# Performance work log

Measured on AMD Instinct MI355X. Metric: run time of the kernel, lower is better.

Reference implementation:

```python
import math
import jax, jax.numpy as jnp
import numpy as np

H = 1024          # hidden size
NH = 16           # num attention heads
HD = H // NH      # head dim = 64
MAXPOS = 1024
HYP_W = 0.5


def setup_inputs() -> dict:
    key = jax.random.key(0)
    ks = jax.random.split(key, 9)
    B, S = 4, 1024
    scale = 1.0 / math.sqrt(H)
    return {
        "hidden_states": jax.random.normal(ks[0], (B, S, H), jnp.float32),
        "attention_mask": jnp.zeros((B, 1, 1, S), jnp.float32),
        "hyperbolic_attention_scores": jax.random.normal(ks[1], (B, S, S), jnp.float32),
        "Wq": jax.random.normal(ks[2], (H, H), jnp.float32) * scale,
        "bq": jnp.zeros((H,), jnp.float32),
        "Wk": jax.random.normal(ks[3], (H, H), jnp.float32) * scale,
        "bk": jnp.zeros((H,), jnp.float32),
        "Wv": jax.random.normal(ks[4], (H, H), jnp.float32) * scale,
        "bv": jnp.zeros((H,), jnp.float32),
        "dist_emb": jax.random.normal(ks[5], (2 * MAXPOS - 1, HD), jnp.float32) * 0.02,
    }


def reference(hidden_states, attention_mask, hyperbolic_attention_scores,
              Wq, bq, Wk, bk, Wv, bv, dist_emb):
    B, S, _ = hidden_states.shape

    def split_heads(x):  # [B,S,H] -> [B,NH,S,HD]
        return x.reshape(B, S, NH, HD).transpose(0, 2, 1, 3)

    q = split_heads(hidden_states @ Wq + bq)
    k = split_heads(hidden_states @ Wk + bk)
    v = split_heads(hidden_states @ Wv + bv)

    # raw scores [B,NH,Sq,Sk]
    scores = jnp.einsum("bhqd,bhkd->bhqk", q, k)

    # relative_key_query position bias
    distance = jnp.arange(S)[:, None] - jnp.arange(S)[None, :]  # [Sq,Sk]
    pe = dist_emb[distance + MAXPOS - 1]                        # [Sq,Sk,HD]
    scores = scores + jnp.einsum("bhld,lrd->bhlr", q, pe)
    scores = scores + jnp.einsum("bhrd,lrd->bhlr", k, pe)

    scores = scores / math.sqrt(HD)
    scores = scores + HYP_W * hyperbolic_attention_scores[:, None, :, :]
    scores = scores + attention_mask

    probs = jax.nn.softmax(scores, axis=-1)
    ctx = jnp.einsum("bhqk,bhkd->bhqd", probs, v)  # [B,NH,S,HD]
    ctx = ctx.transpose(0, 2, 1, 3).reshape(B, S, H)
    return ctx
```

## Files before the change

kernel.cpp:

```cpp
#include <hip/hip_runtime.h>
#include <math.h>

#define S_SEQ 1024
#define NHEAD 16
#define HDIM  64
#define BATCH 4

typedef __attribute__((ext_vector_type(8))) short bf16x8;
typedef __attribute__((ext_vector_type(4))) float f32x4;

#define MFMA16 __builtin_amdgcn_mfma_f32_16x16x32_bf16

__device__ __forceinline__ float bf2f(unsigned short h) {
    union { unsigned u; float f; } un; un.u = ((unsigned)h) << 16; return un.f;
}
__device__ __forceinline__ unsigned short f2bf(float x) {
    union { float f; unsigned u; } un; un.f = x;
    unsigned r = un.u + 0x7FFFu + ((un.u >> 16) & 1u);
    return (unsigned short)(r >> 16);
}
__device__ __forceinline__ unsigned pack2bf(float a, float b) {
    return (unsigned)f2bf(a) | ((unsigned)f2bf(b) << 16);
}
__device__ __forceinline__ void glds16(const unsigned short* g, unsigned short* l) {
    __builtin_amdgcn_global_load_lds(
        (const __attribute__((address_space(1))) void*)g,
        (__attribute__((address_space(3))) void*)l, 16, 0, 0);
}

#define HS_F4 1048576
#define PE_F4 32752
#define CONV_BLKS ((HS_F4 + PE_F4 + 255) / 256)

__global__ __launch_bounds__(256) void prep_kernel(
    const float* __restrict__ hs, const float* __restrict__ de,
    const float* __restrict__ Wq, const float* __restrict__ Wk,
    const float* __restrict__ Wv,
    unsigned short* __restrict__ hsb, unsigned short* __restrict__ peb,
    unsigned short* __restrict__ wt)
{
    __shared__ float tl[64 * 67];
    const int bx = blockIdx.x;
    const int t = threadIdx.x;

    if (bx < CONV_BLKS) {
        int i = bx * 256 + t;
        if (i < HS_F4) {
            float4 v = ((const float4*)hs)[i];
            uint2 o;
            o.x = pack2bf(v.x, v.y);
            o.y = pack2bf(v.z, v.w);
            *(uint2*)(hsb + 4 * (size_t)i) = o;
        } else if (i < HS_F4 + PE_F4) {
            int j = i - HS_F4;
            float4 v = ((const float4*)de)[j];
            uint2 o;
            o.x = pack2bf(v.x, v.y);
            o.y = pack2bf(v.z, v.w);
            *(uint2*)(peb + 4 * (size_t)j) = o;
        }
        return;
    }

    const int id = bx - CONV_BLKS;
    const int which = id >> 8;
    const int rem = id & 255;
    const float* W = (which == 0) ? Wq : (which == 1) ? Wk : Wv;
    unsigned short* outp = wt + (size_t)which * 1024 * 1024;
    const int k0 = (rem >> 4) * 64, n0 = (rem & 15) * 64;

#pragma unroll
    for (int it = 0; it < 4; ++it) {
        int idx = t + it * 256;
        int kr = idx >> 4;
        int c4 = (idx & 15) << 2;
        float4 v = *(const float4*)(W + (size_t)(k0 + kr) * 1024 + n0 + c4);
        tl[kr * 67 + c4 + 0] = v.x; tl[kr * 67 + c4 + 1] = v.y;
        tl[kr * 67 + c4 + 2] = v.z; tl[kr * 67 + c4 + 3] = v.w;
    }
    __syncthreads();
#pragma unroll
    for (int it = 0; it < 2; ++it) {
        int idx = t + it * 256;
        int nr = idx >> 3;
        int k8 = (idx & 7) << 3;
        unsigned short r[8];
#pragma unroll
        for (int e = 0; e < 8; ++e) r[e] = f2bf(tl[(k8 + e) * 67 + nr]);
        uint4 o;
        o.x = (unsigned)r[0] | ((unsigned)r[1] << 16);
        o.y = (unsigned)r[2] | ((unsigned)r[3] << 16);
        o.z = (unsigned)r[4] | ((unsigned)r[5] << 16);
        o.w = (unsigned)r[6] | ((unsigned)r[7] << 16);
        *(uint4*)(outp + (size_t)(n0 + nr) * 1024 + k0 + k8) = o;
    }
}

__global__ __launch_bounds__(256, 3) void qkv_mfma_kernel(
    const unsigned short* __restrict__ hsb, const unsigned short* __restrict__ wt,
    const float* __restrict__ bq, const float* __restrict__ bk,
    const float* __restrict__ bv,
    unsigned short* __restrict__ qo, unsigned short* __restrict__ ko,
    unsigned short* __restrict__ vo)
{
    __shared__ unsigned short As[128 * 64];
    __shared__ unsigned short Bs[128 * 64];

    const int t = threadIdx.x;
    const int lane = t & 63, w = t >> 6;
    const int l16 = lane & 15, quad = lane >> 4;
    const int wm = w >> 1, wn = w & 1;
    const int lrow = lane >> 3, cs = lane & 7;

    const int lid = blockIdx.x + 8 * blockIdx.y + 256 * blockIdx.z;
    const int x = lid & 7, pos = lid >> 3;
    const int pl = pos / 24, sub = pos - pl * 24;
    const int m0 = (4 * x + pl) * 128;
    const int which = sub >> 3;
    const int n0 = (sub & 7) * 128;

    const unsigned short* wts = wt + (size_t)which * 1024 * 1024;
    const float* bias = (which == 0) ? bq : (which == 1) ? bk : bv;

    f32x4 acc[4][4];
#pragma unroll
    for (int i = 0; i < 4; ++i)
#pragma unroll
        for (int j = 0; j < 4; ++j) acc[i][j] = (f32x4){0.f, 0.f, 0.f, 0.f};

    for (int kk = 0; kk < 1024; kk += 64) {
#pragma unroll
        for (int it = 0; it < 4; ++it) {
            int mrow = 32 * w + 8 * it + lrow;
            int kch = cs ^ (mrow & 7);
            glds16(hsb + (size_t)(m0 + mrow) * 1024 + kk + kch * 8,
                   &As[(32 * w + 8 * it) * 64]);
            glds16(wts + (size_t)(n0 + mrow) * 1024 + kk + kch * 8,
                   &Bs[(32 * w + 8 * it) * 64]);
        }
        __syncthreads();

        bf16x8 af[4][2], bf[4][2];
#pragma unroll
        for (int i = 0; i < 4; ++i) {
            int am = 64 * wm + 16 * i + l16;
            int base = am * 64;
            af[i][0] = *(bf16x8*)&As[base + ((quad ^ (am & 7)) << 3)];
            af[i][1] = *(bf16x8*)&As[base + (((quad + 4) ^ (am & 7)) << 3)];
        }
#pragma unroll
        for (int j = 0; j < 4; ++j) {
            int bn = 64 * wn + 16 * j + l16;
            int base = bn * 64;
            bf[j][0] = *(bf16x8*)&Bs[base + ((quad ^ (bn & 7)) << 3)];
            bf[j][1] = *(bf16x8*)&Bs[base + (((quad + 4) ^ (bn & 7)) << 3)];
        }
#pragma unroll
        for (int i = 0; i < 4; ++i)
#pragma unroll
            for (int j = 0; j < 4; ++j) {
                acc[i][j] = MFMA16(af[i][0], bf[j][0], acc[i][j], 0, 0, 0);
                acc[i][j] = MFMA16(af[i][1], bf[j][1], acc[i][j], 0, 0, 0);
            }
        __syncthreads();
    }

    const float qs = (which == 0) ? 0.125f : 1.0f;
#pragma unroll
    for (int j = 0; j < 4; ++j) {
        int n = n0 + 64 * wn + 16 * j + l16;
        float bvv = bias[n];
        int hh = n >> 6, hd = n & 63;
#pragma unroll
        for (int i = 0; i < 4; ++i) {
            int mb = m0 + 64 * wm + 16 * i + 4 * quad;
            int bb = mb >> 10, s = mb & 1023;
            if (which == 2) {
                uint2 o;
                o.x = pack2bf(acc[i][j][0] + bvv, acc[i][j][1] + bvv);
                o.y = pack2bf(acc[i][j][2] + bvv, acc[i][j][3] + bvv);
                *(uint2*)(vo + ((size_t)(bb * NHEAD + hh) * HDIM + hd) * S_SEQ + s) = o;
            } else {
                unsigned short* outp = (which == 0) ? qo : ko;
#pragma unroll
                for (int r = 0; r < 4; ++r)
                    outp[((size_t)(bb * NHEAD + hh) * S_SEQ + s + r) * HDIM + hd] =
                        f2bf((acc[i][j][r] + bvv) * qs);
            }
        }
    }
}

__global__ __launch_bounds__(256, 4) void attn_mfma_kernel(
    const unsigned short* __restrict__ qw, const unsigned short* __restrict__ kw,
    const unsigned short* __restrict__ vtw, const unsigned short* __restrict__ peb,
    const float* __restrict__ hyp, const float* __restrict__ mask,
    float* __restrict__ out)
{
    __shared__ unsigned short pes[128 * 64];
    __shared__ unsigned short QDs[64 * 100];
    __shared__ unsigned short KDs[96 * 36];
    __shared__ unsigned short ps[64 * 32];

    const int t = threadIdx.x;
    const int lane = t & 63, w = t >> 6;
    const int l16 = lane & 15, quad = lane >> 4;
    const int lL = 16 * w + l16;
    const int l0 = blockIdx.x * 64;
    const int h = blockIdx.y, b = blockIdx.z;

    const unsigned short* qb = qw + ((size_t)(b * NHEAD + h) * S_SEQ + l0) * HDIM;
    const unsigned short* kb = kw + (size_t)(b * NHEAD + h) * S_SEQ * HDIM;
    const unsigned short* vtb = vtw + (size_t)(b * NHEAD + h) * HDIM * S_SEQ;
    const float* hypb = hyp + (size_t)b * S_SEQ * S_SEQ + (size_t)(l0 + lL) * S_SEQ;
    const float* maskb = mask + b * S_SEQ;

    const bf16x8 qf0 = *(const bf16x8*)(qb + lL * 64 + quad * 8);
    const bf16x8 qf1 = *(const bf16x8*)(qb + lL * 64 + 32 + quad * 8);

    const int pb0 = l0 + 992;
    int sbP = pb0 & 127;
    int sbQ = pb0 % 96;
    int cQ = (pb0 - lL) % 96;

    const int strow = t >> 3, stp = t & 7;
    const int swzl = (lL >> 1) & 3;

    const int fstart = (w < 2) ? 3 * w : 2 * w + 2;
    const int fcnt   = (w < 2) ? 3 : 2;

    f32x4 accO[4];
#pragma unroll
    for (int jf = 0; jf < 4; ++jf) accO[jf] = (f32x4){0.f, 0.f, 0.f, 0.f};
    float m_run = -INFINITY, lsum = 0.f;

#pragma unroll
    for (int it = 0; it < 2; ++it) {
        int idx = t + it * 256;
        int row = idx >> 3, p = idx & 7;
        int ar = pb0 + 32 + row;
        int slot = ar & 127;
        int src = ar > 2046 ? 2046 : ar;
        *(uint4*)&pes[slot * 64 + (p << 3)] =
            *(const uint4*)(peb + (size_t)src * 64 + ((p ^ (ar & 7)) << 3));
    }
    __syncthreads();

#pragma unroll
    for (int jd = 0; jd < 4; ++jd) {
        int s = (sbP + 32 + 16 * jd + l16) & 127;
        const int sw = s & 7;
        bf16x8 p0 = *(bf16x8*)&pes[s * 64 + ((quad ^ sw) << 3)];
        bf16x8 p1 = *(bf16x8*)&pes[s * 64 + (((quad + 4) ^ sw) << 3)];
        f32x4 aq = (f32x4){0.f, 0.f, 0.f, 0.f};
        aq = MFMA16(p0, qf0, aq, 0, 0, 0);
        aq = MFMA16(p1, qf1, aq, 0, 0, 0);
        int cb = cQ + 32 + 16 * jd + 4 * quad;
#pragma unroll
        for (int i = 0; i < 4; ++i) {
            int c = cb + i; if (c >= 96) c -= 96;
            QDs[lL * 100 + c] = f2bf(aq[i]);
        }
    }

    bf16x8 kfC0 = *(const bf16x8*)(kb + (size_t)l16 * 64 + quad * 8);
    bf16x8 kfC1 = *(const bf16x8*)(kb + (size_t)l16 * 64 + 32 + quad * 8);
    bf16x8 kfC2 = *(const bf16x8*)(kb + (size_t)(16 + l16) * 64 + quad * 8);
    bf16x8 kfC3 = *(const bf16x8*)(kb + (size_t)(16 + l16) * 64 + 32 + quad * 8);
    uint4 peReg;
    {
        int ar = pb0 + strow;
        peReg = *(const uint4*)(peb + (size_t)ar * 64 + ((stp ^ (ar & 7)) << 3));
    }

    for (int kt = 0; kt < 32; ++kt) {
        const int r0 = 32 * kt;

        const float4 hv0 = *(const float4*)(hypb + r0 + 4 * quad);
        const float4 hv1 = *(const float4*)(hypb + r0 + 16 + 4 * quad);
        const float4 mv0 = *(const float4*)(maskb + r0 + 4 * quad);
        const float4 mv1 = *(const float4*)(maskb + r0 + 16 + 4 * quad);

        {
            int slot = (sbP + strow) & 127;
            *(uint4*)&pes[slot * 64 + (stp << 3)] = peReg;
        }
        __syncthreads();

        __builtin_amdgcn_s_setprio(1);
        f32x4 accS0 = (f32x4){0.f, 0.f, 0.f, 0.f};
        f32x4 accS1 = (f32x4){0.f, 0.f, 0.f, 0.f};
        accS0 = MFMA16(kfC0, qf0, accS0, 0, 0, 0);
        accS0 = MFMA16(kfC1, qf1, accS0, 0, 0, 0);
        accS1 = MFMA16(kfC2, qf0, accS1, 0, 0, 0);
        accS1 = MFMA16(kfC3, qf1, accS1, 0, 0, 0);

#pragma unroll
        for (int jd = 0; jd < 2; ++jd) {
            int s = (sbP + 16 * jd + l16) & 127;
            const int sw = s & 7;
            bf16x8 p0 = *(bf16x8*)&pes[s * 64 + ((quad ^ sw) << 3)];
            bf16x8 p1 = *(bf16x8*)&pes[s * 64 + (((quad + 4) ^ sw) << 3)];
            f32x4 aq = (f32x4){0.f, 0.f, 0.f, 0.f};
            aq = MFMA16(p0, qf0, aq, 0, 0, 0);
            aq = MFMA16(p1, qf1, aq, 0, 0, 0);
            int cb = cQ + 16 * jd + 4 * quad;
#pragma unroll
            for (int i = 0; i < 4; ++i) {
                int c = cb + i; if (c >= 96) c -= 96;
                QDs[lL * 100 + c] = f2bf(aq[i]);
            }
        }

#pragma unroll
        for (int jk = 0; jk < 3; ++jk) {
            if (jk < fcnt) {
                const int f = fstart + jk;
                const int diB = 16 * ((f + 1) >> 1);
                const int rB = (f & 1) ? 0 : 16;
                int s = (sbP + diB + l16) & 127;
                const int sw = s & 7;
                bf16x8 p0 = *(bf16x8*)&pes[s * 64 + ((quad ^ sw) << 3)];
                bf16x8 p1 = *(bf16x8*)&pes[s * 64 + (((quad + 4) ^ sw) << 3)];
                f32x4 ak = (f32x4){0.f, 0.f, 0.f, 0.f};
                if (rB == 0) {
                    ak = MFMA16(p0, kfC0, ak, 0, 0, 0);
                    ak = MFMA16(p1, kfC1, ak, 0, 0, 0);
                } else {
                    ak = MFMA16(p0, kfC2, ak, 0, 0, 0);
                    ak = MFMA16(p1, kfC3, ak, 0, 0, 0);
                }
                const int colr = rB + l16;
                const int aB = diB + colr + 4 * quad - 16;
#pragma unroll
                for (int i = 0; i < 4; ++i)
                    KDs[(aB + i) * 36 + colr] = f2bf(ak[i] * 0.125f);
            }
        }
        __builtin_amdgcn_s_setprio(0);
        __syncthreads();

        {
            const int r0n = (kt < 31) ? r0 + 32 : r0;
            kfC0 = *(const bf16x8*)(kb + (size_t)(r0n + l16) * 64 + quad * 8);
            kfC1 = *(const bf16x8*)(kb + (size_t)(r0n + l16) * 64 + 32 + quad * 8);
            kfC2 = *(const bf16x8*)(kb + (size_t)(r0n + 16 + l16) * 64 + quad * 8);
            kfC3 = *(const bf16x8*)(kb + (size_t)(r0n + 16 + l16) * 64 + 32 + quad * 8);
            int ar = pb0 - r0n + strow;
            peReg = *(const uint4*)(peb + (size_t)ar * 64 + ((stp ^ (ar & 7)) << 3));
        }
        bf16x8 vvA[4];
#pragma unroll
        for (int jf = 0; jf < 4; ++jf)
            vvA[jf] = *(const bf16x8*)(vtb + (size_t)(16 * jf + l16) * S_SEQ +
                                       r0 + quad * 8);

        float sc0[4], sc1[4];
        {
            uint2 qd2 = *(uint2*)&QDs[lL * 100 + sbQ + 28 - 4 * quad];
            uint2 kd2 = *(uint2*)&KDs[(lL + 15) * 36 + 4 * quad];
            float hm0 = fmaf(0.5f, hv0.x, mv0.x);
            float hm1 = fmaf(0.5f, hv0.y, mv0.y);
            float hm2 = fmaf(0.5f, hv0.z, mv0.z);
            float hm3 = fmaf(0.5f, hv0.w, mv0.w);
            sc0[0] = accS0[0] + bf2f((unsigned short)(qd2.y >> 16)) +
                     bf2f((unsigned short)(kd2.x & 0xffff)) + hm0;
            sc0[1] = accS0[1] + bf2f((unsigned short)(qd2.y & 0xffff)) +
                     bf2f((unsigned short)(kd2.x >> 16)) + hm1;
            sc0[2] = accS0[2] + bf2f((unsigned short)(qd2.x >> 16)) +
                     bf2f((unsigned short)(kd2.y & 0xffff)) + hm2;
            sc0[3] = accS0[3] + bf2f((unsigned short)(qd2.x & 0xffff)) +
                     bf2f((unsigned short)(kd2.y >> 16)) + hm3;
        }
        {
            uint2 qd2 = *(uint2*)&QDs[lL * 100 + sbQ + 12 - 4 * quad];
            uint2 kd2 = *(uint2*)&KDs[(lL + 15) * 36 + 16 + 4 * quad];
            float hm0 = fmaf(0.5f, hv1.x, mv1.x);
            float hm1 = fmaf(0.5f, hv1.y, mv1.y);
            float hm2 = fmaf(0.5f, hv1.z, mv1.z);
            float hm3 = fmaf(0.5f, hv1.w, mv1.w);
            sc1[0] = accS1[0] + bf2f((unsigned short)(qd2.y >> 16)) +
                     bf2f((unsigned short)(kd2.x & 0xffff)) + hm0;
            sc1[1] = accS1[1] + bf2f((unsigned short)(qd2.y & 0xffff)) +
                     bf2f((unsigned short)(kd2.x >> 16)) + hm1;
            sc1[2] = accS1[2] + bf2f((unsigned short)(qd2.x >> 16)) +
                     bf2f((unsigned short)(kd2.y & 0xffff)) + hm2;
            sc1[3] = accS1[3] + bf2f((unsigned short)(qd2.x & 0xffff)) +
                     bf2f((unsigned short)(kd2.y >> 16)) + hm3;
        }

        float mx = fmaxf(fmaxf(fmaxf(sc0[0], sc0[1]), fmaxf(sc0[2], sc0[3])),
                         fmaxf(fmaxf(sc1[0], sc1[1]), fmaxf(sc1[2], sc1[3])));
        mx = fmaxf(mx, __shfl_xor(mx, 16));
        mx = fmaxf(mx, __shfl_xor(mx, 32));
        const float m_new = fmaxf(m_run, mx);
        const float al = __expf(m_run - m_new);
        m_run = m_new;
        float rs = 0.f;
#pragma unroll
        for (int i = 0; i < 4; ++i) { sc0[i] = __expf(sc0[i] - m_new); rs += sc0[i]; }
#pragma unroll
        for (int i = 0; i < 4; ++i) { sc1[i] = __expf(sc1[i] - m_new); rs += sc1[i]; }
        rs += __shfl_xor(rs, 16);
        rs += __shfl_xor(rs, 32);
        lsum = lsum * al + rs;

        {
            uint2 pw;
            pw.x = pack2bf(sc0[0], sc0[1]); pw.y = pack2bf(sc0[2], sc0[3]);
            *(uint2*)&ps[lL * 32 + (((quad >> 1) ^ swzl) << 3) + 4 * (quad & 1)] = pw;
            pw.x = pack2bf(sc1[0], sc1[1]); pw.y = pack2bf(sc1[2], sc1[3]);
            *(uint2*)&ps[lL * 32 + (((2 + (quad >> 1)) ^ swzl) << 3) + 4 * (quad & 1)] = pw;
        }

        const bf16x8 pf = *(const bf16x8*)&ps[lL * 32 + ((quad ^ swzl) << 3)];
        const float alv0 = __shfl(al, 4 * quad + 0);
        const float alv1 = __shfl(al, 4 * quad + 1);
        const float alv2 = __shfl(al, 4 * quad + 2);
        const float alv3 = __shfl(al, 4 * quad + 3);
#pragma unroll
        for (int jf = 0; jf < 4; ++jf) {
            f32x4 o = accO[jf];
            o[0] *= alv0; o[1] *= alv1; o[2] *= alv2; o[3] *= alv3;
            o = MFMA16(pf, vvA[jf], o, 0, 0, 0);
            accO[jf] = o;
        }

        sbP = (sbP - 32) & 127;
        sbQ -= 32; if (sbQ < 0) sbQ += 96;
        cQ -= 32; if (cQ < 0) cQ += 96;
    }

    const float ls0 = __shfl(lsum, 4 * quad + 0);
    const float ls1 = __shfl(lsum, 4 * quad + 1);
    const float ls2 = __shfl(lsum, 4 * quad + 2);
    const float ls3 = __shfl(lsum, 4 * quad + 3);
#pragma unroll
    for (int jf = 0; jf < 4; ++jf) {
        const size_t col = (size_t)h * 64 + 16 * jf + l16;
        float* ob = out + ((size_t)b * S_SEQ + l0 + 16 * w + 4 * quad) * 1024 + col;
        ob[0]        = accO[jf][0] / ls0;
        ob[1024]     = accO[jf][1] / ls1;
        ob[2048]     = accO[jf][2] / ls2;
        ob[3072]     = accO[jf][3] / ls3;
    }
}

extern "C" void kernel_launch(void* const* d_in, const int* in_sizes, int n_in,
                              void* d_out, int out_size, void* d_ws, size_t ws_size,
                              hipStream_t stream) {
    const float* hs   = (const float*)d_in[0];
    const float* mask = (const float*)d_in[1];
    const float* hyp  = (const float*)d_in[2];
    const float* Wq   = (const float*)d_in[3];
    const float* bq   = (const float*)d_in[4];
    const float* Wk   = (const float*)d_in[5];
    const float* bk   = (const float*)d_in[6];
    const float* Wv   = (const float*)d_in[7];
    const float* bv   = (const float*)d_in[8];
    const float* de   = (const float*)d_in[9];

    char* ws = (char*)d_ws;
    unsigned short* qw  = (unsigned short*)(ws);
    unsigned short* kw  = (unsigned short*)(ws + (8u << 20));
    unsigned short* vtw = (unsigned short*)(ws + (16u << 20));
    unsigned short* hsb = (unsigned short*)(ws + (24u << 20));
    unsigned short* wt  = (unsigned short*)(ws + (32u << 20));
    unsigned short* peb = (unsigned short*)(ws + (38u << 20));

    prep_kernel<<<dim3(CONV_BLKS + 768), 256, 0, stream>>>(hs, de, Wq, Wk, Wv,
                                                           hsb, peb, wt);
    qkv_mfma_kernel<<<dim3(8, 32, 3), 256, 0, stream>>>(hsb, wt, bq, bk, bv, qw, kw, vtw);
    attn_mfma_kernel<<<dim3(16, NHEAD, BATCH), 256, 0, stream>>>(
        qw, kw, vtw, peb, hyp, mask, (float*)d_out);
}
```

Measured before the change: 288.3 us.

## Use per-wave KD buffers to drop a barrier and prefetch next-tile operands

The shared KD tile becomes a private buffer per wave, and each wave computes all four key-distance fragments it needs itself. This removes the second __syncthreads per iteration at the cost of redundant MFMA work across waves. The hyperbolic/mask, V and PE loads are moved one iteration ahead so their latency overlaps compute. Launch bounds drop from 4 to 3 blocks per SM to make room for the extra registers, which may lower occupancy.

Result: slower. 298.0 us (+3.3%).

```diff
diff --git a/kernel.cpp b/kernel.cpp
--- a/kernel.cpp
+++ b/kernel.cpp
@@ -191,7 +191,7 @@
     }
 }
 
-__global__ __launch_bounds__(256, 4) void attn_mfma_kernel(
+__global__ __launch_bounds__(256, 3) void attn_mfma_kernel(
     const unsigned short* __restrict__ qw, const unsigned short* __restrict__ kw,
     const unsigned short* __restrict__ vtw, const unsigned short* __restrict__ peb,
     const float* __restrict__ hyp, const float* __restrict__ mask,
@@ -199,7 +199,7 @@
 {
     __shared__ unsigned short pes[128 * 64];
     __shared__ unsigned short QDs[64 * 100];
-    __shared__ unsigned short KDs[96 * 36];
+    __shared__ unsigned short KDw[4][48 * 36];
     __shared__ unsigned short ps[64 * 32];
 
     const int t = threadIdx.x;
@@ -225,9 +225,6 @@
 
     const int strow = t >> 3, stp = t & 7;
     const int swzl = (lL >> 1) & 3;
-
-    const int fstart = (w < 2) ? 3 * w : 2 * w + 2;
-    const int fcnt   = (w < 2) ? 3 : 2;
 
     f32x4 accO[4];
 #pragma unroll
@@ -272,20 +269,29 @@
         int ar = pb0 + strow;
         peReg = *(const uint4*)(peb + (size_t)ar * 64 + ((stp ^ (ar & 7)) << 3));
     }
+    float4 hv0 = *(const float4*)(hypb + 4 * quad);
+    float4 hv1 = *(const float4*)(hypb + 16 + 4 * quad);
+    float4 mv0 = *(const float4*)(maskb + 4 * quad);
+    float4 mv1 = *(const float4*)(maskb + 16 + 4 * quad);
+    bf16x8 vvA[4];
+#pragma unroll
+    for (int jf = 0; jf < 4; ++jf)
+        vvA[jf] = *(const bf16x8*)(vtb + (size_t)(16 * jf + l16) * S_SEQ + quad * 8);
 
     for (int kt = 0; kt < 32; ++kt) {
         const int r0 = 32 * kt;
-
-        const float4 hv0 = *(const float4*)(hypb + r0 + 4 * quad);
-        const float4 hv1 = *(const float4*)(hypb + r0 + 16 + 4 * quad);
-        const float4 mv0 = *(const float4*)(maskb + r0 + 4 * quad);
-        const float4 mv1 = *(const float4*)(maskb + r0 + 16 + 4 * quad);
+        const int r0n = (kt < 31) ? r0 + 32 : r0;
 
         {
             int slot = (sbP + strow) & 127;
             *(uint4*)&pes[slot * 64 + (stp << 3)] = peReg;
         }
         __syncthreads();
+
+        {
+            int ar = pb0 - r0n + strow;
+            peReg = *(const uint4*)(peb + (size_t)ar * 64 + ((stp ^ (ar & 7)) << 3));
+        }
 
         __builtin_amdgcn_s_setprio(1);
         f32x4 accS0 = (f32x4){0.f, 0.f, 0.f, 0.f};
@@ -313,52 +319,38 @@
         }
 
 #pragma unroll
-        for (int jk = 0; jk < 3; ++jk) {
-            if (jk < fcnt) {
-                const int f = fstart + jk;
-                const int diB = 16 * ((f + 1) >> 1);
-                const int rB = (f & 1) ? 0 : 16;
-                int s = (sbP + diB + l16) & 127;
-                const int sw = s & 7;
-                bf16x8 p0 = *(bf16x8*)&pes[s * 64 + ((quad ^ sw) << 3)];
-                bf16x8 p1 = *(bf16x8*)&pes[s * 64 + (((quad + 4) ^ sw) << 3)];
-                f32x4 ak = (f32x4){0.f, 0.f, 0.f, 0.f};
-                if (rB == 0) {
-                    ak = MFMA16(p0, kfC0, ak, 0, 0, 0);
-                    ak = MFMA16(p1, kfC1, ak, 0, 0, 0);
-                } else {
-                    ak = MFMA16(p0, kfC2, ak, 0, 0, 0);
-                    ak = MFMA16(p1, kfC3, ak, 0, 0, 0);
-                }
-                const int colr = rB + l16;
-                const int aB = diB + colr + 4 * quad - 16;
-#pragma unroll
-                for (int i = 0; i < 4; ++i)
-                    KDs[(aB + i) * 36 + colr] = f2bf(ak[i] * 0.125f);
+        for (int f = 0; f < 4; ++f) {
+            const int diBp = (f == 0) ? 16 : (f == 1) ? 32 : (f == 2) ? 0 : 16;
+            const int rB = (f < 2) ? 0 : 16;
+            int s = (sbP + 16 * w + diBp + l16) & 127;
+            const int sw = s & 7;
+            bf16x8 p0 = *(bf16x8*)&pes[s * 64 + ((quad ^ sw) << 3)];
+            bf16x8 p1 = *(bf16x8*)&pes[s * 64 + (((quad + 4) ^ sw) << 3)];
+            f32x4 ak = (f32x4){0.f, 0.f, 0.f, 0.f};
+            if (rB == 0) {
+                ak = MFMA16(p0, kfC0, ak, 0, 0, 0);
+                ak = MFMA16(p1, kfC1, ak, 0, 0, 0);
+            } else {
+                ak = MFMA16(p0, kfC2, ak, 0, 0, 0);
+                ak = MFMA16(p1, kfC3, ak, 0, 0, 0);
             }
+            const int colr = rB + l16;
+            const int rL = diBp + 4 * quad + colr - 16;
+#pragma unroll
+            for (int i = 0; i < 4; ++i)
+                KDw[w][(rL + i) * 36 + colr] = f2bf(ak[i] * 0.125f);
         }
         __builtin_amdgcn_s_setprio(0);
-        __syncthreads();
-
-        {
-            const int r0n = (kt < 31) ? r0 + 32 : r0;
-            kfC0 = *(const bf16x8*)(kb + (size_t)(r0n + l16) * 64 + quad * 8);
-            kfC1 = *(const bf16x8*)(kb + (size_t)(r0n + l16) * 64 + 32 + quad * 8);
-            kfC2 = *(const bf16x8*)(kb + (size_t)(r0n + 16 + l16) * 64 + quad * 8);
-            kfC3 = *(const bf16x8*)(kb + (size_t)(r0n + 16 + l16) * 64 + 32 + quad * 8);
-            int ar = pb0 - r0n + strow;
-            peReg = *(const uint4*)(peb + (size_t)ar * 64 + ((stp ^ (ar & 7)) << 3));
-        }
-        bf16x8 vvA[4];
-#pragma unroll
-        for (int jf = 0; jf < 4; ++jf)
-            vvA[jf] = *(const bf16x8*)(vtb + (size_t)(16 * jf + l16) * S_SEQ +
-                                       r0 + quad * 8);
+
+        kfC0 = *(const bf16x8*)(kb + (size_t)(r0n + l16) * 64 + quad * 8);
+        kfC1 = *(const bf16x8*)(kb + (size_t)(r0n + l16) * 64 + 32 + quad * 8);
+        kfC2 = *(const bf16x8*)(kb + (size_t)(r0n + 16 + l16) * 64 + quad * 8);
+        kfC3 = *(const bf16x8*)(kb + (size_t)(r0n + 16 + l16) * 64 + 32 + quad * 8);
 
         float sc0[4], sc1[4];
         {
             uint2 qd2 = *(uint2*)&QDs[lL * 100 + sbQ + 28 - 4 * quad];
-            uint2 kd2 = *(uint2*)&KDs[(lL + 15) * 36 + 4 * quad];
+            uint2 kd2 = *(uint2*)&KDw[w][(l16 + 15) * 36 + 4 * quad];
             float hm0 = fmaf(0.5f, hv0.x, mv0.x);
             float hm1 = fmaf(0.5f, hv0.y, mv0.y);
             float hm2 = fmaf(0.5f, hv0.z, mv0.z);
@@ -374,7 +366,7 @@
         }
         {
             uint2 qd2 = *(uint2*)&QDs[lL * 100 + sbQ + 12 - 4 * quad];
-            uint2 kd2 = *(uint2*)&KDs[(lL + 15) * 36 + 16 + 4 * quad];
+            uint2 kd2 = *(uint2*)&KDw[w][(l16 + 15) * 36 + 16 + 4 * quad];
             float hm0 = fmaf(0.5f, hv1.x, mv1.x);
             float hm1 = fmaf(0.5f, hv1.y, mv1.y);
             float hm2 = fmaf(0.5f, hv1.z, mv1.z);
@@ -389,6 +381,11 @@
                      bf2f((unsigned short)(kd2.y >> 16)) + hm3;
         }
 
+        hv0 = *(const float4*)(hypb + r0n + 4 * quad);
+        hv1 = *(const float4*)(hypb + r0n + 16 + 4 * quad);
+        mv0 = *(const float4*)(maskb + r0n + 4 * quad);
+        mv1 = *(const float4*)(maskb + r0n + 16 + 4 * quad);
+
         float mx = fmaxf(fmaxf(fmaxf(sc0[0], sc0[1]), fmaxf(sc0[2], sc0[3])),
                          fmaxf(fmaxf(sc1[0], sc1[1]), fmaxf(sc1[2], sc1[3])));
         mx = fmaxf(mx, __shfl_xor(mx, 16));
@@ -425,6 +422,11 @@
             o = MFMA16(pf, vvA[jf], o, 0, 0, 0);
             accO[jf] = o;
         }
+
+#pragma unroll
+        for (int jf = 0; jf < 4; ++jf)
+            vvA[jf] = *(const bf16x8*)(vtb + (size_t)(16 * jf + l16) * S_SEQ +
+                                       r0n + quad * 8);
 
         sbP = (sbP - 32) & 127;
         sbQ -= 32; if (sbQ < 0) sbQ += 96;
```

## Drop shared PE ring buffer; load PE rows directly and use per-wave KD tiles

Applied to the files above, without the earlier changes.

Removes the block-shared positional-embedding ring buffer and its staging. Each wave now loads the PE rows it needs straight from global memory (L1/L2 cached) into registers. The key-distance tile is made per-wave, with each wave computing all four fragments it needs, so both __syncthreads per iteration are gone. The cost is redundant MFMA work and more global/L2 traffic for PE rows, in exchange for no block-wide barriers and less LDS use. The lower LDS footprint may allow higher occupancy.

New measurement: 534.6 us. 85.4% more time.

```diff
diff --git a/kernel.cpp b/kernel.cpp
--- a/kernel.cpp
+++ b/kernel.cpp
@@ -197,9 +197,8 @@
     const float* __restrict__ hyp, const float* __restrict__ mask,
     float* __restrict__ out)
 {
-    __shared__ unsigned short pes[128 * 64];
     __shared__ unsigned short QDs[64 * 100];
-    __shared__ unsigned short KDs[96 * 36];
+    __shared__ unsigned short KDw[4][17 * 36];
     __shared__ unsigned short ps[64 * 32];
 
     const int t = threadIdx.x;
@@ -219,15 +218,10 @@
     const bf16x8 qf1 = *(const bf16x8*)(qb + lL * 64 + 32 + quad * 8);
 
     const int pb0 = l0 + 992;
-    int sbP = pb0 & 127;
     int sbQ = pb0 % 96;
     int cQ = (pb0 - lL) % 96;
 
-    const int strow = t >> 3, stp = t & 7;
     const int swzl = (lL >> 1) & 3;
-
-    const int fstart = (w < 2) ? 3 * w : 2 * w + 2;
-    const int fcnt   = (w < 2) ? 3 : 2;
 
     f32x4 accO[4];
 #pragma unroll
@@ -235,23 +229,11 @@
     float m_run = -INFINITY, lsum = 0.f;
 
 #pragma unroll
-    for (int it = 0; it < 2; ++it) {
-        int idx = t + it * 256;
-        int row = idx >> 3, p = idx & 7;
-        int ar = pb0 + 32 + row;
-        int slot = ar & 127;
-        int src = ar > 2046 ? 2046 : ar;
-        *(uint4*)&pes[slot * 64 + (p << 3)] =
-            *(const uint4*)(peb + (size_t)src * 64 + ((p ^ (ar & 7)) << 3));
-    }
-    __syncthreads();
-
-#pragma unroll
     for (int jd = 0; jd < 4; ++jd) {
-        int s = (sbP + 32 + 16 * jd + l16) & 127;
-        const int sw = s & 7;
-        bf16x8 p0 = *(bf16x8*)&pes[s * 64 + ((quad ^ sw) << 3)];
-        bf16x8 p1 = *(bf16x8*)&pes[s * 64 + (((quad + 4) ^ sw) << 3)];
+        int row = pb0 + 32 + 16 * jd + l16;
+        int src = row > 2046 ? 2046 : row;
+        bf16x8 p0 = *(const bf16x8*)(peb + (size_t)src * 64 + quad * 8);
+        bf16x8 p1 = *(const bf16x8*)(peb + (size_t)src * 64 + 32 + quad * 8);
         f32x4 aq = (f32x4){0.f, 0.f, 0.f, 0.f};
         aq = MFMA16(p0, qf0, aq, 0, 0, 0);
         aq = MFMA16(p1, qf1, aq, 0, 0, 0);
@@ -267,25 +249,38 @@
     bf16x8 kfC1 = *(const bf16x8*)(kb + (size_t)l16 * 64 + 32 + quad * 8);
     bf16x8 kfC2 = *(const bf16x8*)(kb + (size_t)(16 + l16) * 64 + quad * 8);
     bf16x8 kfC3 = *(const bf16x8*)(kb + (size_t)(16 + l16) * 64 + 32 + quad * 8);
-    uint4 peReg;
-    {
-        int ar = pb0 + strow;
-        peReg = *(const uint4*)(peb + (size_t)ar * 64 + ((stp ^ (ar & 7)) << 3));
-    }
 
     for (int kt = 0; kt < 32; ++kt) {
         const int r0 = 32 * kt;
-
+        const int pb = pb0 - r0;
+        const int r0n = (kt < 31) ? r0 + 32 : r0;
+
+        bf16x8 qdA[2][2];
+#pragma unroll
+        for (int jd = 0; jd < 2; ++jd) {
+            const size_t rowb = (size_t)(pb + 16 * jd + l16) * 64;
+            qdA[jd][0] = *(const bf16x8*)(peb + rowb + quad * 8);
+            qdA[jd][1] = *(const bf16x8*)(peb + rowb + 32 + quad * 8);
+        }
+        bf16x8 kdA[4][2];
+#pragma unroll
+        for (int f = 0; f < 4; ++f) {
+            const int diBp = (f == 0) ? 16 : (f == 1) ? 32 : (f == 2) ? 0 : 16;
+            int row = pb + 16 * w + diBp + l16;
+            if (row > 2046) row = 2046;
+            const size_t rowb = (size_t)row * 64;
+            kdA[f][0] = *(const bf16x8*)(peb + rowb + quad * 8);
+            kdA[f][1] = *(const bf16x8*)(peb + rowb + 32 + quad * 8);
+        }
         const float4 hv0 = *(const float4*)(hypb + r0 + 4 * quad);
         const float4 hv1 = *(const float4*)(hypb + r0 + 16 + 4 * quad);
         const float4 mv0 = *(const float4*)(maskb + r0 + 4 * quad);
         const float4 mv1 = *(const float4*)(maskb + r0 + 16 + 4 * quad);
-
-        {
-            int slot = (sbP + strow) & 127;
-            *(uint4*)&pes[slot * 64 + (stp << 3)] = peReg;
-        }
-        __syncthreads();
+        bf16x8 vvA[4];
+#pragma unroll
+        for (int jf = 0; jf < 4; ++jf)
+            vvA[jf] = *(const bf16x8*)(vtb + (size_t)(16 * jf + l16) * S_SEQ +
+                                       r0 + quad * 8);
 
         __builtin_amdgcn_s_setprio(1);
         f32x4 accS0 = (f32x4){0.f, 0.f, 0.f, 0.f};
@@ -297,13 +292,9 @@
 
 #pragma unroll
         for (int jd = 0; jd < 2; ++jd) {
-            int s = (sbP + 16 * jd + l16) & 127;
-            const int sw = s & 7;
-            bf16x8 p0 = *(bf16x8*)&pes[s * 64 + ((quad ^ sw) << 3)];
-            bf16x8 p1 = *(bf16x8*)&pes[s * 64 + (((quad + 4) ^ sw) << 3)];
             f32x4 aq = (f32x4){0.f, 0.f, 0.f, 0.f};
-            aq = MFMA16(p0, qf0, aq, 0, 0, 0);
-            aq = MFMA16(p1, qf1, aq, 0, 0, 0);
+            aq = MFMA16(qdA[jd][0], qf0, aq, 0, 0, 0);
+            aq = MFMA16(qdA[jd][1], qf1, aq, 0, 0, 0);
             int cb = cQ + 16 * jd + 4 * quad;
 #pragma unroll
             for (int i = 0; i < 4; ++i) {
@@ -313,52 +304,37 @@
         }
 
 #pragma unroll
-        for (int jk = 0; jk < 3; ++jk) {
-            if (jk < fcnt) {
-                const int f = fstart + jk;
-                const int diB = 16 * ((f + 1) >> 1);
-                const int rB = (f & 1) ? 0 : 16;
-                int s = (sbP + diB + l16) & 127;
-                const int sw = s & 7;
-                bf16x8 p0 = *(bf16x8*)&pes[s * 64 + ((quad ^ sw) << 3)];
-                bf16x8 p1 = *(bf16x8*)&pes[s * 64 + (((quad + 4) ^ sw) << 3)];
-                f32x4 ak = (f32x4){0.f, 0.f, 0.f, 0.f};
-                if (rB == 0) {
-                    ak = MFMA16(p0, kfC0, ak, 0, 0, 0);
-                    ak = MFMA16(p1, kfC1, ak, 0, 0, 0);
-                } else {
-                    ak = MFMA16(p0, kfC2, ak, 0, 0, 0);
-                    ak = MFMA16(p1, kfC3, ak, 0, 0, 0);
-                }
-                const int colr = rB + l16;
-                const int aB = diB + colr + 4 * quad - 16;
-#pragma unroll
-                for (int i = 0; i < 4; ++i)
-                    KDs[(aB + i) * 36 + colr] = f2bf(ak[i] * 0.125f);
+        for (int f = 0; f < 4; ++f) {
+            const int diBp = (f == 0) ? 16 : (f == 1) ? 32 : (f == 2) ? 0 : 16;
+            const int rB = (f < 2) ? 0 : 16;
+            f32x4 ak = (f32x4){0.f, 0.f, 0.f, 0.f};
+            if (rB == 0) {
+                ak = MFMA16(kdA[f][0], kfC0, ak, 0, 0, 0);
+                ak = MFMA16(kdA[f][1], kfC1, ak, 0, 0, 0);
+            } else {
+                ak = MFMA16(kdA[f][0], kfC2, ak, 0, 0, 0);
+                ak = MFMA16(kdA[f][1], kfC3, ak, 0, 0, 0);
             }
+            const int colr = rB + l16;
+            const int rbase = diBp + 4 * quad + colr - 31;
+#pragma unroll
+            for (int i = 0; i < 4; ++i) {
+                unsigned rr = (unsigned)(rbase + i);
+                rr = rr < 16u ? rr : 16u;
+                KDw[w][rr * 36 + colr] = f2bf(ak[i] * 0.125f);
+            }
         }
         __builtin_amdgcn_s_setprio(0);
-        __syncthreads();
-
-        {
-            const int r0n = (kt < 31) ? r0 + 32 : r0;
-            kfC0 = *(const bf16x8*)(kb + (size_t)(r0n + l16) * 64 + quad * 8);
-            kfC1 = *(const bf16x8*)(kb + (size_t)(r0n + l16) * 64 + 32 + quad * 8);
-            kfC2 = *(const bf16x8*)(kb + (size_t)(r0n + 16 + l16) * 64 + quad * 8);
-            kfC3 = *(const bf16x8*)(kb + (size_t)(r0n + 16 + l16) * 64 + 32 + quad * 8);
-            int ar = pb0 - r0n + strow;
-            peReg = *(const uint4*)(peb + (size_t)ar * 64 + ((stp ^ (ar & 7)) << 3));
-        }
-        bf16x8 vvA[4];
-#pragma unroll
-        for (int jf = 0; jf < 4; ++jf)
-            vvA[jf] = *(const bf16x8*)(vtb + (size_t)(16 * jf + l16) * S_SEQ +
-                                       r0 + quad * 8);
+
+        kfC0 = *(const bf16x8*)(kb + (size_t)(r0n + l16) * 64 + quad * 8);
+        kfC1 = *(const bf16x8*)(kb + (size_t)(r0n + l16) * 64 + 32 + quad * 8);
+        kfC2 = *(const bf16x8*)(kb + (size_t)(r0n + 16 + l16) * 64 + quad * 8);
+        kfC3 = *(const bf16x8*)(kb + (size_t)(r0n + 16 + l16) * 64 + 32 + quad * 8);
 
         float sc0[4], sc1[4];
         {
             uint2 qd2 = *(uint2*)&QDs[lL * 100 + sbQ + 28 - 4 * quad];
-            uint2 kd2 = *(uint2*)&KDs[(lL + 15) * 36 + 4 * quad];
+            uint2 kd2 = *(uint2*)&KDw[w][l16 * 36 + 4 * quad];
             float hm0 = fmaf(0.5f, hv0.x, mv0.x);
             float hm1 = fmaf(0.5f, hv0.y, mv0.y);
             float hm2 = fmaf(0.5f, hv0.z, mv0.z);
@@ -374,7 +350,7 @@
         }
         {
             uint2 qd2 = *(uint2*)&QDs[lL * 100 + sbQ + 12 - 4 * quad];
-            uint2 kd2 = *(uint2*)&KDs[(lL + 15) * 36 + 16 + 4 * quad];
+            uint2 kd2 = *(uint2*)&KDw[w][l16 * 36 + 16 + 4 * quad];
             float hm0 = fmaf(0.5f, hv1.x, mv1.x);
             float hm1 = fmaf(0.5f, hv1.y, mv1.y);
             float hm2 = fmaf(0.5f, hv1.z, mv1.z);
@@ -426,7 +402,6 @@
             accO[jf] = o;
         }
 
-        sbP = (sbP - 32) & 127;
         sbQ -= 32; if (sbQ < 0) sbQ += 96;
         cQ -= 32; if (cQ < 0) cQ += 96;
     }
```

## Split attention over two key halves and merge partials in a combine kernel

Applied to the files above, without the earlier changes.

Doubles the attention grid by assigning each block half of the key range, writing unnormalized bf16 partial outputs plus running max and sum. A new combine kernel rescales and merges the two halves into the final fp32 output. This aims to increase parallelism and shorten per-block serial loops. The cost is extra global traffic for the partials, an extra launch, a duplicated prologue, and bf16 rounding of the partial outputs.

Result: slower. 312.6 us (+8.4%).

```diff
diff --git a/kernel.cpp b/kernel.cpp
--- a/kernel.cpp
+++ b/kernel.cpp
@@ -5,6 +5,7 @@
 #define NHEAD 16
 #define HDIM  64
 #define BATCH 4
+#define TOTROW (BATCH * NHEAD * S_SEQ)
 
 typedef __attribute__((ext_vector_type(8))) short bf16x8;
 typedef __attribute__((ext_vector_type(4))) float f32x4;
@@ -22,6 +23,8 @@
 __device__ __forceinline__ unsigned pack2bf(float a, float b) {
     return (unsigned)f2bf(a) | ((unsigned)f2bf(b) << 16);
 }
+__device__ __forceinline__ float bflo(unsigned u) { return bf2f((unsigned short)(u & 0xffff)); }
+__device__ __forceinline__ float bfhi(unsigned u) { return bf2f((unsigned short)(u >> 16)); }
 __device__ __forceinline__ void glds16(const unsigned short* g, unsigned short* l) {
     __builtin_amdgcn_global_load_lds(
         (const __attribute__((address_space(1))) void*)g,
@@ -195,7 +198,8 @@
     const unsigned short* __restrict__ qw, const unsigned short* __restrict__ kw,
     const unsigned short* __restrict__ vtw, const unsigned short* __restrict__ peb,
     const float* __restrict__ hyp, const float* __restrict__ mask,
-    float* __restrict__ out)
+    unsigned short* __restrict__ po, float* __restrict__ mw,
+    float* __restrict__ lw)
 {
     __shared__ unsigned short pes[128 * 64];
     __shared__ unsigned short QDs[64 * 100];
@@ -206,7 +210,9 @@
     const int lane = t & 63, w = t >> 6;
     const int l16 = lane & 15, quad = lane >> 4;
     const int lL = 16 * w + l16;
-    const int l0 = blockIdx.x * 64;
+    const int qtile = blockIdx.x & 15, khalf = blockIdx.x >> 4;
+    const int l0 = qtile * 64;
+    const int r_base = khalf * 512;
     const int h = blockIdx.y, b = blockIdx.z;
 
     const unsigned short* qb = qw + ((size_t)(b * NHEAD + h) * S_SEQ + l0) * HDIM;
@@ -218,10 +224,11 @@
     const bf16x8 qf0 = *(const bf16x8*)(qb + lL * 64 + quad * 8);
     const bf16x8 qf1 = *(const bf16x8*)(qb + lL * 64 + 32 + quad * 8);
 
-    const int pb0 = l0 + 992;
+    const int pb0 = l0 + 992 - r_base;
     int sbP = pb0 & 127;
     int sbQ = pb0 % 96;
     int cQ = (pb0 - lL) % 96;
+    if (cQ < 0) cQ += 96;
 
     const int strow = t >> 3, stp = t & 7;
     const int swzl = (lL >> 1) & 3;
@@ -263,18 +270,19 @@
         }
     }
 
-    bf16x8 kfC0 = *(const bf16x8*)(kb + (size_t)l16 * 64 + quad * 8);
-    bf16x8 kfC1 = *(const bf16x8*)(kb + (size_t)l16 * 64 + 32 + quad * 8);
-    bf16x8 kfC2 = *(const bf16x8*)(kb + (size_t)(16 + l16) * 64 + quad * 8);
-    bf16x8 kfC3 = *(const bf16x8*)(kb + (size_t)(16 + l16) * 64 + 32 + quad * 8);
+    bf16x8 kfC0 = *(const bf16x8*)(kb + (size_t)(r_base + l16) * 64 + quad * 8);
+    bf16x8 kfC1 = *(const bf16x8*)(kb + (size_t)(r_base + l16) * 64 + 32 + quad * 8);
+    bf16x8 kfC2 = *(const bf16x8*)(kb + (size_t)(r_base + 16 + l16) * 64 + quad * 8);
+    bf16x8 kfC3 = *(const bf16x8*)(kb + (size_t)(r_base + 16 + l16) * 64 + 32 + quad * 8);
     uint4 peReg;
     {
         int ar = pb0 + strow;
         peReg = *(const uint4*)(peb + (size_t)ar * 64 + ((stp ^ (ar & 7)) << 3));
     }
 
-    for (int kt = 0; kt < 32; ++kt) {
-        const int r0 = 32 * kt;
+    for (int kt = 0; kt < 16; ++kt) {
+        const int rr = 32 * kt;
+        const int r0 = r_base + rr;
 
         const float4 hv0 = *(const float4*)(hypb + r0 + 4 * quad);
         const float4 hv1 = *(const float4*)(hypb + r0 + 16 + 4 * quad);
@@ -341,12 +349,13 @@
         __syncthreads();
 
         {
-            const int r0n = (kt < 31) ? r0 + 32 : r0;
+            const int rrn = (kt < 15) ? rr + 32 : rr;
+            const int r0n = r_base + rrn;
             kfC0 = *(const bf16x8*)(kb + (size_t)(r0n + l16) * 64 + quad * 8);
             kfC1 = *(const bf16x8*)(kb + (size_t)(r0n + l16) * 64 + 32 + quad * 8);
             kfC2 = *(const bf16x8*)(kb + (size_t)(r0n + 16 + l16) * 64 + quad * 8);
             kfC3 = *(const bf16x8*)(kb + (size_t)(r0n + 16 + l16) * 64 + 32 + quad * 8);
-            int ar = pb0 - r0n + strow;
+            int ar = pb0 - rrn + strow;
             peReg = *(const uint4*)(peb + (size_t)ar * 64 + ((stp ^ (ar & 7)) << 3));
         }
         bf16x8 vvA[4];
@@ -363,14 +372,10 @@
             float hm1 = fmaf(0.5f, hv0.y, mv0.y);
             float hm2 = fmaf(0.5f, hv0.z, mv0.z);
             float hm3 = fmaf(0.5f, hv0.w, mv0.w);
-            sc0[0] = accS0[0] + bf2f((unsigned short)(qd2.y >> 16)) +
-                     bf2f((unsigned short)(kd2.x & 0xffff)) + hm0;
-            sc0[1] = accS0[1] + bf2f((unsigned short)(qd2.y & 0xffff)) +
-                     bf2f((unsigned short)(kd2.x >> 16)) + hm1;
-            sc0[2] = accS0[2] + bf2f((unsigned short)(qd2.x >> 16)) +
-                     bf2f((unsigned short)(kd2.y & 0xffff)) + hm2;
-            sc0[3] = accS0[3] + bf2f((unsigned short)(qd2.x & 0xffff)) +
-                     bf2f((unsigned short)(kd2.y >> 16)) + hm3;
+            sc0[0] = accS0[0] + bfhi(qd2.y) + bflo(kd2.x) + hm0;
+            sc0[1] = accS0[1] + bflo(qd2.y) + bfhi(kd2.x) + hm1;
+            sc0[2] = accS0[2] + bfhi(qd2.x) + bflo(kd2.y) + hm2;
+            sc0[3] = accS0[3] + bflo(qd2.x) + bfhi(kd2.y) + hm3;
         }
         {
             uint2 qd2 = *(uint2*)&QDs[lL * 100 + sbQ + 12 - 4 * quad];
@@ -379,14 +384,10 @@
             float hm1 = fmaf(0.5f, hv1.y, mv1.y);
             float hm2 = fmaf(0.5f, hv1.z, mv1.z);
             float hm3 = fmaf(0.5f, hv1.w, mv1.w);
-            sc1[0] = accS1[0] + bf2f((unsigned short)(qd2.y >> 16)) +
-                     bf2f((unsigned short)(kd2.x & 0xffff)) + hm0;
-            sc1[1] = accS1[1] + bf2f((unsigned short)(qd2.y & 0xffff)) +
-                     bf2f((unsigned short)(kd2.x >> 16)) + hm1;
-            sc1[2] = accS1[2] + bf2f((unsigned short)(qd2.x >> 16)) +
-                     bf2f((unsigned short)(kd2.y & 0xffff)) + hm2;
-            sc1[3] = accS1[3] + bf2f((unsigned short)(qd2.x & 0xffff)) +
-                     bf2f((unsigned short)(kd2.y >> 16)) + hm3;
+            sc1[0] = accS1[0] + bfhi(qd2.y) + bflo(kd2.x) + hm0;
+            sc1[1] = accS1[1] + bflo(qd2.y) + bfhi(kd2.x) + hm1;
+            sc1[2] = accS1[2] + bfhi(qd2.x) + bflo(kd2.y) + hm2;
+            sc1[3] = accS1[3] + bflo(qd2.x) + bfhi(kd2.y) + hm3;
         }
 
         float mx = fmaxf(fmaxf(fmaxf(sc0[0], sc0[1]), fmaxf(sc0[2], sc0[3])),
@@ -431,19 +432,54 @@
         cQ -= 32; if (cQ < 0) cQ += 96;
     }
 
-    const float ls0 = __shfl(lsum, 4 * quad + 0);
-    const float ls1 = __shfl(lsum, 4 * quad + 1);
-    const float ls2 = __shfl(lsum, 4 * quad + 2);
-    const float ls3 = __shfl(lsum, 4 * quad + 3);
+    unsigned short* pob = po + (size_t)khalf * TOTROW * 64 +
+                          ((size_t)(b * NHEAD + h) * S_SEQ + l0) * 64;
 #pragma unroll
     for (int jf = 0; jf < 4; ++jf) {
-        const size_t col = (size_t)h * 64 + 16 * jf + l16;
-        float* ob = out + ((size_t)b * S_SEQ + l0 + 16 * w + 4 * quad) * 1024 + col;
-        ob[0]        = accO[jf][0] / ls0;
-        ob[1024]     = accO[jf][1] / ls1;
-        ob[2048]     = accO[jf][2] / ls2;
-        ob[3072]     = accO[jf][3] / ls3;
-    }
+        const int col = 16 * jf + l16;
+#pragma unroll
+        for (int i = 0; i < 4; ++i)
+            pob[(size_t)(16 * w + 4 * quad + i) * 64 + col] = f2bf(accO[jf][i]);
+    }
+    if (quad == 0) {
+        size_t mi = (size_t)khalf * TOTROW + (size_t)(b * NHEAD + h) * S_SEQ + l0 + lL;
+        mw[mi] = m_run;
+        lw[mi] = lsum;
+    }
+}
+
+__global__ __launch_bounds__(256) void combine_kernel(
+    const unsigned short* __restrict__ po, const float* __restrict__ mw,
+    const float* __restrict__ lw, float* __restrict__ out)
+{
+    const int tid = blockIdx.x * 256 + threadIdx.x;
+    const int d8 = tid & 7, row = tid >> 3;
+    const int bb = row >> 14, hh = (row >> 10) & 15, s = row & 1023;
+
+    const float m0 = mw[row], m1 = mw[row + TOTROW];
+    const float l0 = lw[row], l1 = lw[row + TOTROW];
+    const float M = fmaxf(m0, m1);
+    float a0 = __expf(m0 - M), a1 = __expf(m1 - M);
+    const float inv = 1.0f / fmaf(a0, l0, a1 * l1);
+    a0 *= inv; a1 *= inv;
+
+    const unsigned short* p0 = po + (size_t)row * 64 + d8 * 8;
+    const uint4 u0 = *(const uint4*)p0;
+    const uint4 u1 = *(const uint4*)(p0 + (size_t)TOTROW * 64);
+
+    float4 r0, r1;
+    r0.x = a0 * bflo(u0.x) + a1 * bflo(u1.x);
+    r0.y = a0 * bfhi(u0.x) + a1 * bfhi(u1.x);
+    r0.z = a0 * bflo(u0.y) + a1 * bflo(u1.y);
+    r0.w = a0 * bfhi(u0.y) + a1 * bfhi(u1.y);
+    r1.x = a0 * bflo(u0.z) + a1 * bflo(u1.z);
+    r1.y = a0 * bfhi(u0.z) + a1 * bfhi(u1.z);
+    r1.z = a0 * bflo(u0.w) + a1 * bflo(u1.w);
+    r1.w = a0 * bfhi(u0.w) + a1 * bfhi(u1.w);
+
+    float* ob = out + ((size_t)bb * S_SEQ + s) * 1024 + hh * 64 + d8 * 8;
+    *(float4*)ob = r0;
+    *(float4*)(ob + 4) = r1;
 }
 
 extern "C" void kernel_launch(void* const* d_in, const int* in_sizes, int n_in,
@@ -467,10 +503,14 @@
     unsigned short* hsb = (unsigned short*)(ws + (24u << 20));
     unsigned short* wt  = (unsigned short*)(ws + (32u << 20));
     unsigned short* peb = (unsigned short*)(ws + (38u << 20));
+    unsigned short* po  = (unsigned short*)(ws + (39u << 20));
+    float*          mwp = (float*)(ws + (55u << 20));
+    float*          lwp = (float*)(ws + (55u << 20) + (1u << 19));
 
     prep_kernel<<<dim3(CONV_BLKS + 768), 256, 0, stream>>>(hs, de, Wq, Wk, Wv,
                                                            hsb, peb, wt);
     qkv_mfma_kernel<<<dim3(8, 32, 3), 256, 0, stream>>>(hsb, wt, bq, bk, bv, qw, kw, vtw);
-    attn_mfma_kernel<<<dim3(16, NHEAD, BATCH), 256, 0, stream>>>(
-        qw, kw, vtw, peb, hyp, mask, (float*)d_out);
-}
+    attn_mfma_kernel<<<dim3(32, NHEAD, BATCH), 256, 0, stream>>>(
+        qw, kw, vtw, peb, hyp, mask, po, mwp, lwp);
+    combine_kernel<<<dim3(2048), 256, 0, stream>>>(po, mwp, lwp, (float*)d_out);
+}
```
